# Performance work log

Measured on AMD Instinct MI355X. Metric: run time of the kernel, lower is better.

## Reference

```python
import jax, jax.numpy as jnp
import numpy as np

B, S, D_MODEL, D_FF, E, K = 4, 2048, 1024, 4096, 8, 2
CAP_FACTOR = 1.0


def setup_inputs() -> dict:
    key = jax.random.key(0)
    ks = jax.random.split(key, 6)
    std = 0.02
    return {
        "x": jax.random.normal(ks[0], (B, S, D_MODEL), jnp.float32),
        "router_w": jax.random.normal(ks[1], (E, D_MODEL), jnp.float32) * std,  # Linear(d_model,E,bias=False) weight
        "w1": jax.random.normal(ks[2], (E, D_MODEL, D_FF), jnp.float32) * std,
        "b1": jnp.zeros((E, D_FF), jnp.float32),
        "w2": jax.random.normal(ks[3], (E, D_FF, D_MODEL), jnp.float32) * std,
        "b2": jnp.zeros((E, D_MODEL), jnp.float32),
    }


def reference(x, router_w, w1, b1, w2, b2):
    b, s, d = x.shape
    T = b * s
    e = router_w.shape[0]
    capacity = int(CAP_FACTOR * T / e)  # static
    xf = x.reshape(T, d)

    # --- routing ---
    logits = xf @ router_w.T                       # [T,E]
    probs = jax.nn.softmax(logits, axis=-1)
    vals, idx = jax.lax.top_k(probs, K)            # [T,K] values / expert ids
    vals = vals / vals.sum(-1, keepdims=True)

    # dense gate matrix [T,E]; top_k experts are distinct so this is a scatter of K weights per token
    ar = jnp.arange(T)
    gates = jnp.zeros((T, e), x.dtype).at[ar[:, None], idx].add(vals)

    # --- load-balancing loss ---
    counts = jnp.zeros((e,), jnp.float32).at[idx.reshape(-1)].add(1.0)
    ideal = T * K / e
    lb_loss = jnp.sum((counts - ideal) ** 2) / (T ** 2)

    # --- capacity-limited dispatch (first `capacity` tokens in token order per expert) ---
    mask = gates > 0                                               # [T,E]
    order = jnp.argsort(jnp.logical_not(mask), axis=0)[:capacity]  # stable: assigned tokens first, ascending token id -> [cap,E]
    valid = jnp.take_along_axis(mask, order, axis=0)               # [cap,E] token actually assigned & within capacity
    idx_ec = order.T                                               # [E,cap]

    # --- grouped expert MLP ---
    xg = xf[idx_ec]                                                # [E,cap,D]
    h = jax.nn.gelu(jnp.einsum('ecd,edf->ecf', xg, w1) + b1[:, None, :], approximate=False)
    y = jnp.einsum('ecf,efd->ecd', h, w2) + b2[:, None, :]         # [E,cap,D]

    # --- combine (scatter-add with routing weights; dropped/invalid slots get weight 0) ---
    wt = gates[idx_ec, jnp.arange(e)[:, None]] * valid.T           # [E,cap]
    out = jnp.zeros((T, d), x.dtype).at[idx_ec.reshape(-1)].add((y * wt[..., None]).reshape(-1, d))
    return out.reshape(b, s, d), lb_loss
```

## Files before the change

### kernel.cpp

```cpp
#include <hip/hip_runtime.h>
#include <hip/hip_bf16.h>

#define T_TOK 8192
#define DMODEL 1024
#define DFF 4096
#define NEXP 8
#define CAP 1024

typedef __attribute__((ext_vector_type(8))) __bf16 bf16x8;
typedef __attribute__((ext_vector_type(4))) float f32x4;

__device__ __forceinline__ unsigned short f2bf(float f) {
  union { float f; unsigned int u; } v;
  v.f = f;
  return (unsigned short)((v.u + 0x7fffu + ((v.u >> 16) & 1u)) >> 16);
}

__device__ __forceinline__ float bfbits2f(unsigned int lo16) {
  union { unsigned int u; float f; } v; v.u = lo16 << 16; return v.f;
}

__device__ __forceinline__ float fast_gelu(float v) {
  float x = fabsf(v) * 0.70710678118654752440f;
  float t = __builtin_amdgcn_rcpf(1.0f + 0.3275911f * x);
  float poly = t * (0.254829592f + t * (-0.284496736f + t * (1.421413741f +
               t * (-1.453152027f + t * 1.061405429f))));
  float er = 1.0f - poly * __expf(-x * x);
  float s = (v >= 0.0f) ? er : -er;
  return 0.5f * v * (1.0f + s);
}

__device__ __forceinline__ void load_lds16(const unsigned short* g, unsigned short* l) {
  __builtin_amdgcn_global_load_lds((const __attribute__((address_space(1))) void*)g,
                                   (__attribute__((address_space(3))) void*)l,
                                   16, 0, 0);
}

__global__ void k_router(const float* __restrict__ x, const float* __restrict__ rw,
                         unsigned short* __restrict__ xb,
                         int* __restrict__ tk_idx, float* __restrict__ tk_w,
                         int* __restrict__ tinv) {
  if (threadIdx.x < 8) tinv[blockIdx.x * 8 + threadIdx.x] = -1;
  int wv = threadIdx.x >> 6, lane = threadIdx.x & 63;
  int t = blockIdx.x * 4 + wv;
  const float4* xr = (const float4*)(x + (size_t)t * DMODEL);
  uint2* xbw = (uint2*)(xb + (size_t)t * DMODEL);
  float acc[NEXP];
#pragma unroll
  for (int e = 0; e < NEXP; ++e) acc[e] = 0.f;
#pragma unroll
  for (int j = 0; j < DMODEL / 256; ++j) {
    float4 v = xr[j * 64 + lane];
#pragma unroll
    for (int e = 0; e < NEXP; ++e) {
      float4 w = ((const float4*)(rw + e * DMODEL))[j * 64 + lane];
      acc[e] += v.x * w.x + v.y * w.y + v.z * w.z + v.w * w.w;
    }
    uint2 p;
    p.x = (unsigned int)f2bf(v.x) | ((unsigned int)f2bf(v.y) << 16);
    p.y = (unsigned int)f2bf(v.z) | ((unsigned int)f2bf(v.w) << 16);
    xbw[j * 64 + lane] = p;
  }
#pragma unroll
  for (int e = 0; e < NEXP; ++e)
    for (int off = 32; off; off >>= 1) acc[e] += __shfl_xor(acc[e], off);
  if (lane == 0) {
    int i0 = 0;
    for (int e = 1; e < NEXP; ++e) if (acc[e] > acc[i0]) i0 = e;
    int i1 = (i0 == 0) ? 1 : 0;
    for (int e = 0; e < NEXP; ++e) if (e != i0 && acc[e] > acc[i1]) i1 = e;
    float ex = expf(acc[i1] - acc[i0]);
    float w0 = 1.f / (1.f + ex);
    float w1 = ex / (1.f + ex);
    tk_idx[2 * t] = i0; tk_idx[2 * t + 1] = i1;
    tk_w[2 * t] = w0;  tk_w[2 * t + 1] = w1;
  }
}

__global__ void k_transpose_cvt(const float* __restrict__ src, unsigned short* __restrict__ dst,
                                int Kd, int Nd) {
  __shared__ unsigned short tile[64][73];
  int e = blockIdx.z;
  size_t k0 = (size_t)blockIdx.y * 64, n0 = (size_t)blockIdx.x * 64;
  int tid = threadIdx.x;
  const float* sb = src + (size_t)e * Kd * Nd;
  int r = tid >> 4, cg = (tid & 15) * 4;
  for (int rr = 0; rr < 4; ++rr) {
    int row = r + rr * 16;
    float4 v = *(const float4*)(sb + (k0 + row) * Nd + n0 + cg);
    tile[row][cg + 0] = f2bf(v.x);
    tile[row][cg + 1] = f2bf(v.y);
    tile[row][cg + 2] = f2bf(v.z);
    tile[row][cg + 3] = f2bf(v.w);
  }
  __syncthreads();
  unsigned short* db = dst + (size_t)e * Nd * Kd;
  int rn = tid >> 3, kg = (tid & 7) * 8;
  for (int rr = 0; rr < 2; ++rr) {
    int nrow = rn + rr * 32;
    union { unsigned short h[8]; uint4 v; } o;
#pragma unroll
    for (int j = 0; j < 8; ++j) o.h[j] = tile[kg + j][nrow];
    *(uint4*)(db + (n0 + nrow) * Kd + k0 + kg) = o.v;
  }
}

__global__ void k_scan(const int* __restrict__ tk_idx, const float* __restrict__ tk_w,
                       int* __restrict__ etok, float* __restrict__ egate,
                       int* __restrict__ tinv, int* __restrict__ counts) {
  __shared__ int wavecnt[8][16];
  __shared__ int waveoff[8][16];
  int e = blockIdx.x;
  int tid = threadIdx.x, lane = tid & 63, wv = tid >> 6;
  for (int i = tid; i < CAP; i += 1024) etok[e * CAP + i] = 0;
  unsigned long long lt = (1ULL << lane) - 1ULL;
  int pos[8], wh[8];
  bool mine[8];
#pragma unroll
  for (int c = 0; c < 8; ++c) {
    int t = c * 1024 + tid;
    int e0 = tk_idx[2 * t], e1 = tk_idx[2 * t + 1];
    bool is0 = (e0 == e), is1 = (e1 == e);
    mine[c] = is0 || is1;
    wh[c] = is1 ? 1 : 0;
    unsigned long long bal = __ballot(mine[c]);
    pos[c] = __popcll(bal & lt);
    if (lane == 0) wavecnt[c][wv] = __popcll(bal);
  }
  __syncthreads();
  if (tid == 0) {
    int s = 0;
    for (int c = 0; c < 8; ++c)
      for (int w = 0; w < 16; ++w) { waveoff[c][w] = s; s += wavecnt[c][w]; }
    counts[e] = s;
  }
  __syncthreads();
#pragma unroll
  for (int c = 0; c < 8; ++c) {
    if (mine[c]) {
      int t = c * 1024 + tid;
      int r = waveoff[c][wv] + pos[c];
      if (r < CAP) {
        etok[e * CAP + r] = t;
        egate[e * CAP + r] = tk_w[2 * t + wh[c]];
        tinv[2 * t + wh[c]] = e * CAP + r;
      }
    }
  }
}

__global__ __launch_bounds__(256) void k_gemm1(
    const unsigned short* __restrict__ xb, const unsigned short* __restrict__ w1t,
    const float* __restrict__ b1, const int* __restrict__ etok,
    unsigned short* __restrict__ H) {
  __shared__ __align__(16) unsigned short smem[16384];
  int tid = threadIdx.x;
  int lane = tid & 63, wv = tid >> 6;
  int bid = blockIdx.x;
  int e = bid >> 8;
  int b = bid & 255;
  int nl = b & 7, m = (b >> 3) & 7, nh = b >> 6;
  int m0 = m * 128, n0 = (nh * 8 + nl) * 128;

  const unsigned short* gA[2];
  const unsigned short* gB[2];
  int wb[2];
#pragma unroll
  for (int s = 0; s < 2; ++s) {
    int i = s * 256 + tid;
    int row = i >> 2;
    int q = (i & 3) ^ ((i >> 3) & 3);
    int tok = etok[e * CAP + m0 + row];
    gA[s] = xb + (size_t)tok * DMODEL + q * 8;
    gB[s] = w1t + ((size_t)e * DFF + n0 + row) * DMODEL + q * 8;
    wb[s] = (s * 256 + wv * 64) * 8;
  }

  f32x4 zero = {0.f, 0.f, 0.f, 0.f};
  f32x4 acc[4][4];
#pragma unroll
  for (int mi = 0; mi < 4; ++mi)
#pragma unroll
    for (int ni = 0; ni < 4; ++ni) acc[mi][ni] = zero;

  int wm = (wv >> 1) * 64, wn = (wv & 1) * 64;
  int fr = lane & 15, quad = lane >> 4;
  int cs = (quad ^ ((fr >> 1) & 3)) * 8;
  int aoff = (wm + fr) * 32 + cs;
  int boff = (wn + fr) * 32 + cs;

#pragma unroll
  for (int s = 0; s < 2; ++s) {
    load_lds16(gA[s], smem + wb[s]);
    load_lds16(gB[s], smem + 4096 + wb[s]);
  }
  int buf = 0;
  for (int k0 = 32; k0 <= DMODEL; k0 += 32) {
    __syncthreads();
    int nbuf = buf ^ 8192;
    if (k0 < DMODEL) {
#pragma unroll
      for (int s = 0; s < 2; ++s) {
        load_lds16(gA[s] + k0, smem + nbuf + wb[s]);
        load_lds16(gB[s] + k0, smem + nbuf + 4096 + wb[s]);
      }
    }
    const unsigned short* Ab = smem + buf;
    const unsigned short* Bb = Ab + 4096;
    bf16x8 av[4], bv[4];
#pragma unroll
    for (int mi = 0; mi < 4; ++mi) av[mi] = *(const bf16x8*)(Ab + aoff + mi * 512);
#pragma unroll
    for (int ni = 0; ni < 4; ++ni) bv[ni] = *(const bf16x8*)(Bb + boff + ni * 512);
#pragma unroll
    for (int mi = 0; mi < 4; ++mi)
#pragma unroll
      for (int ni = 0; ni < 4; ++ni)
        acc[mi][ni] = __builtin_amdgcn_mfma_f32_16x16x32_bf16(bv[ni], av[mi], acc[mi][ni], 0, 0, 0);
    buf = nbuf;
  }
  __syncthreads();

  unsigned short* EP = smem + wv * 1536;
#pragma unroll
  for (int ni = 0; ni < 4; ++ni) {
    float4 b4 = *(const float4*)(b1 + e * DFF + n0 + wn + ni * 16 + quad * 4);
#pragma unroll
    for (int mi = 0; mi < 4; ++mi) {
      float v0 = fast_gelu(acc[mi][ni][0] + b4.x);
      float v1 = fast_gelu(acc[mi][ni][1] + b4.y);
      float v2 = fast_gelu(acc[mi][ni][2] + b4.z);
      float v3 = fast_gelu(acc[mi][ni][3] + b4.w);
      uint2 p;
      p.x = (unsigned int)f2bf(v0) | ((unsigned int)f2bf(v1) << 16);
      p.y = (unsigned int)f2bf(v2) | ((unsigned int)f2bf(v3) << 16);
      *(uint2*)(EP + (mi * 16 + fr) * 24 + quad * 4) = p;
    }
#pragma unroll
    for (int t = 0; t < 2; ++t) {
      int row = t * 32 + (lane >> 1), chunk = lane & 1;
      uint4 v = *(const uint4*)(EP + row * 24 + chunk * 8);
      *(uint4*)(H + ((size_t)e * CAP + m0 + wm + row) * DFF + n0 + wn + ni * 16 + chunk * 8) = v;
    }
  }
}

__global__ __launch_bounds__(256) void k_gemm2(
    const unsigned short* __restrict__ H, const unsigned short* __restrict__ w2t,
    const float* __restrict__ b2, unsigned short* __restrict__ Y) {
  __shared__ __align__(16) unsigned short smem[16384];
  int tid = threadIdx.x;
  int lane = tid & 63, wv = tid >> 6;
  int bid = blockIdx.x;
  int e = bid & 7;
  int r = bid >> 3;
  int n0 = (r & 7) * 128;
  int m0 = (r >> 3) * 128;

  const unsigned short* gA[2];
  const unsigned short* gB[2];
  int wb[2];
#pragma unroll
  for (int s = 0; s < 2; ++s) {
    int i = s * 256 + tid;
    int row = i >> 2;
    int q = (i & 3) ^ ((i >> 3) & 3);
    gA[s] = H + ((size_t)e * CAP + m0 + row) * DFF + q * 8;
    gB[s] = w2t + ((size_t)e * DMODEL + n0 + row) * DFF + q * 8;
    wb[s] = (s * 256 + wv * 64) * 8;
  }

  f32x4 zero = {0.f, 0.f, 0.f, 0.f};
  f32x4 acc[4][4];
#pragma unroll
  for (int mi = 0; mi < 4; ++mi)
#pragma unroll
    for (int ni = 0; ni < 4; ++ni) acc[mi][ni] = zero;

  int wm = (wv >> 1) * 64, wn = (wv & 1) * 64;
  int fr = lane & 15, quad = lane >> 4;
  int cs = (quad ^ ((fr >> 1) & 3)) * 8;
  int aoff = (wm + fr) * 32 + cs;
  int boff = (wn + fr) * 32 + cs;

#pragma unroll
  for (int s = 0; s < 2; ++s) {
    load_lds16(gA[s], smem + wb[s]);
    load_lds16(gB[s], smem + 4096 + wb[s]);
  }
  int buf = 0;
  for (int k0 = 32; k0 <= DFF; k0 += 32) {
    __syncthreads();
    int nbuf = buf ^ 8192;
    if (k0 < DFF) {
#pragma unroll
      for (int s = 0; s < 2; ++s) {
        load_lds16(gA[s] + k0, smem + nbuf + wb[s]);
        load_lds16(gB[s] + k0, smem + nbuf + 4096 + wb[s]);
      }
    }
    const unsigned short* Ab = smem + buf;
    const unsigned short* Bb = Ab + 4096;
    bf16x8 av[4], bv[4];
#pragma unroll
    for (int mi = 0; mi < 4; ++mi) av[mi] = *(const bf16x8*)(Ab + aoff + mi * 512);
#pragma unroll
    for (int ni = 0; ni < 4; ++ni) bv[ni] = *(const bf16x8*)(Bb + boff + ni * 512);
#pragma unroll
    for (int mi = 0; mi < 4; ++mi)
#pragma unroll
      for (int ni = 0; ni < 4; ++ni)
        acc[mi][ni] = __builtin_amdgcn_mfma_f32_16x16x32_bf16(bv[ni], av[mi], acc[mi][ni], 0, 0, 0);
    buf = nbuf;
  }
  __syncthreads();

  unsigned short* EP = smem + wv * 1536;
#pragma unroll
  for (int ni = 0; ni < 4; ++ni) {
    float4 b4 = *(const float4*)(b2 + e * DMODEL + n0 + wn + ni * 16 + quad * 4);
#pragma unroll
    for (int mi = 0; mi < 4; ++mi) {
      uint2 p;
      p.x = (unsigned int)f2bf(acc[mi][ni][0] + b4.x) |
            ((unsigned int)f2bf(acc[mi][ni][1] + b4.y) << 16);
      p.y = (unsigned int)f2bf(acc[mi][ni][2] + b4.z) |
            ((unsigned int)f2bf(acc[mi][ni][3] + b4.w) << 16);
      *(uint2*)(EP + (mi * 16 + fr) * 24 + quad * 4) = p;
    }
#pragma unroll
    for (int t = 0; t < 2; ++t) {
      int row = t * 32 + (lane >> 1), chunk = lane & 1;
      uint4 v = *(const uint4*)(EP + row * 24 + chunk * 8);
      *(uint4*)(Y + ((size_t)e * CAP + m0 + wm + row) * DMODEL + n0 + wn + ni * 16 + chunk * 8) = v;
    }
  }
}

__global__ void k_combine(const unsigned short* __restrict__ Y,
                          const float* __restrict__ egate,
                          const int* __restrict__ tinv,
                          const int* __restrict__ counts,
                          float* __restrict__ out, float* __restrict__ loss_out) {
  int t = blockIdx.x, tid = threadIdx.x;
  int s0 = tinv[2 * t], s1 = tinv[2 * t + 1];
  int d0 = tid * 4;
  float a0 = 0.f, a1 = 0.f, a2 = 0.f, a3 = 0.f;
  if (s0 >= 0) {
    float g = egate[s0];
    uint2 v = *(const uint2*)(Y + (size_t)s0 * DMODEL + d0);
    a0 += g * bfbits2f(v.x & 0xffff); a1 += g * bfbits2f(v.x >> 16);
    a2 += g * bfbits2f(v.y & 0xffff); a3 += g * bfbits2f(v.y >> 16);
  }
  if (s1 >= 0) {
    float g = egate[s1];
    uint2 v = *(const uint2*)(Y + (size_t)s1 * DMODEL + d0);
    a0 += g * bfbits2f(v.x & 0xffff); a1 += g * bfbits2f(v.x >> 16);
    a2 += g * bfbits2f(v.y & 0xffff); a3 += g * bfbits2f(v.y >> 16);
  }
  float4 o = {a0, a1, a2, a3};
  *(float4*)(out + (size_t)t * DMODEL + d0) = o;
  if (t == 0 && tid == 0) {
    float loss = 0.f;
    for (int e = 0; e < NEXP; ++e) {
      float d = (float)counts[e] - 2048.0f;
      loss += d * d;
    }
    loss_out[0] = loss / (8192.0f * 8192.0f);
  }
}

extern "C" void kernel_launch(void* const* d_in, const int* in_sizes, int n_in,
                              void* d_out, int out_size, void* d_ws, size_t ws_size,
                              hipStream_t stream) {
  (void)in_sizes; (void)n_in; (void)ws_size; (void)out_size;
  const float* x  = (const float*)d_in[0];
  const float* rw = (const float*)d_in[1];
  const float* w1 = (const float*)d_in[2];
  const float* b1 = (const float*)d_in[3];
  const float* w2 = (const float*)d_in[4];
  const float* b2 = (const float*)d_in[5];
  float* out = (float*)d_out;

  char* ws = (char*)d_ws;
  const size_t XB_BYTES = (size_t)T_TOK * DMODEL * 2;
  const size_t WT_BYTES = (size_t)NEXP * DFF * DMODEL * 2;
  const size_t H_BYTES  = (size_t)NEXP * CAP * DFF * 2;
  unsigned short* xb = (unsigned short*)ws;
  unsigned short* Yb = xb;
  unsigned short* wT = (unsigned short*)(ws + XB_BYTES);
  unsigned short* Hb = (unsigned short*)(ws + XB_BYTES + WT_BYTES);
  char* small = ws + XB_BYTES + WT_BYTES + H_BYTES;
  int*   etok   = (int*)small;
  float* egate  = (float*)(small + NEXP * CAP * 4);
  int*   tkidx  = (int*)(small + 2 * NEXP * CAP * 4);
  float* tkw    = (float*)(small + 2 * NEXP * CAP * 4 + T_TOK * 2 * 4);
  int*   tinv   = (int*)(small + 2 * NEXP * CAP * 4 + 2 * T_TOK * 2 * 4);
  int*   counts = (int*)(small + 2 * NEXP * CAP * 4 + 3 * T_TOK * 2 * 4);

  k_router<<<T_TOK / 4, 256, 0, stream>>>(x, rw, xb, tkidx, tkw, tinv);
  k_scan<<<NEXP, 1024, 0, stream>>>(tkidx, tkw, etok, egate, tinv, counts);
  k_transpose_cvt<<<dim3(DFF / 64, DMODEL / 64, NEXP), 256, 0, stream>>>(w1, wT, DMODEL, DFF);
  k_gemm1<<<NEXP * 256, 256, 0, stream>>>(xb, wT, b1, etok, Hb);
  k_transpose_cvt<<<dim3(DMODEL / 64, DFF / 64, NEXP), 256, 0, stream>>>(w2, wT, DFF, DMODEL);
  k_gemm2<<<NEXP * 64, 256, 0, stream>>>(Hb, wT, b2, Yb);
  k_combine<<<T_TOK, 256, 0, stream>>>(Yb, egate, tinv, counts, out,
                                       out + (size_t)T_TOK * DMODEL);
}
```

Before: 544.5 us.

## Triple-buffer LDS in both expert GEMMs with two-stage prefetch

Both expert GEMM kernels move from double-buffered to triple-buffered LDS staging. Global-to-LDS loads are issued two K-tiles ahead, and an explicit vmcnt(4) wait plus a raw s_barrier replaces the per-iteration __syncthreads. The aim is to hide global memory latency behind the MFMA work and avoid draining all outstanding loads every iteration. In exchange, LDS use per block grows by half, which may lower occupancy, and correctness now depends on the hand-tuned vmcnt count matching the number of loads in flight.

```diff
diff --git a/kernel.cpp b/kernel.cpp
--- a/kernel.cpp
+++ b/kernel.cpp
@@ -153,7 +153,7 @@
     const unsigned short* __restrict__ xb, const unsigned short* __restrict__ w1t,
     const float* __restrict__ b1, const int* __restrict__ etok,
     unsigned short* __restrict__ H) {
-  __shared__ __align__(16) unsigned short smem[16384];
+  __shared__ __align__(16) unsigned short smem[24576];
   int tid = threadIdx.x;
   int lane = tid & 63, wv = tid >> 6;
   int bid = blockIdx.x;
@@ -194,18 +194,29 @@
     load_lds16(gA[s], smem + wb[s]);
     load_lds16(gB[s], smem + 4096 + wb[s]);
   }
-  int buf = 0;
-  for (int k0 = 32; k0 <= DMODEL; k0 += 32) {
-    __syncthreads();
-    int nbuf = buf ^ 8192;
-    if (k0 < DMODEL) {
+#pragma unroll
+  for (int s = 0; s < 2; ++s) {
+    load_lds16(gA[s] + 32, smem + 8192 + wb[s]);
+    load_lds16(gB[s] + 32, smem + 8192 + 4096 + wb[s]);
+  }
+
+  const int NT = DMODEL / 32;
+  int cur = 0, stg = 16384;
+  for (int t = 0; t < NT; ++t) {
+    if (t < NT - 1) asm volatile("s_waitcnt vmcnt(4)" ::: "memory");
+    else            asm volatile("s_waitcnt vmcnt(0)" ::: "memory");
+    __builtin_amdgcn_s_barrier();
+    asm volatile("" ::: "memory");
+    if (t + 2 < NT) {
+      int kp = (t + 2) * 32;
 #pragma unroll
       for (int s = 0; s < 2; ++s) {
-        load_lds16(gA[s] + k0, smem + nbuf + wb[s]);
-        load_lds16(gB[s] + k0, smem + nbuf + 4096 + wb[s]);
+        load_lds16(gA[s] + kp, smem + stg + wb[s]);
+        load_lds16(gB[s] + kp, smem + stg + 4096 + wb[s]);
       }
-    }
-    const unsigned short* Ab = smem + buf;
+      stg += 8192; if (stg == 24576) stg = 0;
+    }
+    const unsigned short* Ab = smem + cur;
     const unsigned short* Bb = Ab + 4096;
     bf16x8 av[4], bv[4];
 #pragma unroll
@@ -217,7 +228,7 @@
 #pragma unroll
       for (int ni = 0; ni < 4; ++ni)
         acc[mi][ni] = __builtin_amdgcn_mfma_f32_16x16x32_bf16(bv[ni], av[mi], acc[mi][ni], 0, 0, 0);
-    buf = nbuf;
+    cur += 8192; if (cur == 24576) cur = 0;
   }
   __syncthreads();
 
@@ -248,7 +259,7 @@
 __global__ __launch_bounds__(256) void k_gemm2(
     const unsigned short* __restrict__ H, const unsigned short* __restrict__ w2t,
     const float* __restrict__ b2, unsigned short* __restrict__ Y) {
-  __shared__ __align__(16) unsigned short smem[16384];
+  __shared__ __align__(16) unsigned short smem[24576];
   int tid = threadIdx.x;
   int lane = tid & 63, wv = tid >> 6;
   int bid = blockIdx.x;
@@ -288,18 +299,29 @@
     load_lds16(gA[s], smem + wb[s]);
     load_lds16(gB[s], smem + 4096 + wb[s]);
   }
-  int buf = 0;
-  for (int k0 = 32; k0 <= DFF; k0 += 32) {
-    __syncthreads();
-    int nbuf = buf ^ 8192;
-    if (k0 < DFF) {
+#pragma unroll
+  for (int s = 0; s < 2; ++s) {
+    load_lds16(gA[s] + 32, smem + 8192 + wb[s]);
+    load_lds16(gB[s] + 32, smem + 8192 + 4096 + wb[s]);
+  }
+
+  const int NT = DFF / 32;
+  int cur = 0, stg = 16384;
+  for (int t = 0; t < NT; ++t) {
+    if (t < NT - 1) asm volatile("s_waitcnt vmcnt(4)" ::: "memory");
+    else            asm volatile("s_waitcnt vmcnt(0)" ::: "memory");
+    __builtin_amdgcn_s_barrier();
+    asm volatile("" ::: "memory");
+    if (t + 2 < NT) {
+      int kp = (t + 2) * 32;
 #pragma unroll
       for (int s = 0; s < 2; ++s) {
-        load_lds16(gA[s] + k0, smem + nbuf + wb[s]);
-        load_lds16(gB[s] + k0, smem + nbuf + 4096 + wb[s]);
+        load_lds16(gA[s] + kp, smem + stg + wb[s]);
+        load_lds16(gB[s] + kp, smem + stg + 4096 + wb[s]);
       }
-    }
-    const unsigned short* Ab = smem + buf;
+      stg += 8192; if (stg == 24576) stg = 0;
+    }
+    const unsigned short* Ab = smem + cur;
     const unsigned short* Bb = Ab + 4096;
     bf16x8 av[4], bv[4];
 #pragma unroll
@@ -311,7 +333,7 @@
 #pragma unroll
       for (int ni = 0; ni < 4; ++ni)
         acc[mi][ni] = __builtin_amdgcn_mfma_f32_16x16x32_bf16(bv[ni], av[mi], acc[mi][ni], 0, 0, 0);
-    buf = nbuf;
+    cur += 8192; if (cur == 24576) cur = 0;
   }
   __syncthreads();
 
```

Result: no change. 544.7 us (+0.0%).
